# Optimization experiments

Measured on AMD Instinct MI355X. Metric: run time of the kernel, lower is better.

## Reference

```python
import jax, jax.numpy as jnp
import numpy as np

B, S, D = 2, 1024, 512
G, H, QKD, VD = 8, 8, 64, 64
FFOUT = D

def setup_inputs() -> dict:
    key = jax.random.key(0)
    ks = jax.random.split(key, 7)
    def lin(kw, fan_in, fan_out):
        lim = 1.0 / np.sqrt(fan_in)
        kw1, kw2 = jax.random.split(kw)
        w = jax.random.uniform(kw1, (fan_in, fan_out), jnp.float32, -lim, lim)
        b = jax.random.uniform(kw2, (fan_out,), jnp.float32, -lim, lim)
        return w, b
    x = jax.random.normal(ks[0], (B, S, D), jnp.float32)
    Wq_w, Wq_b = lin(ks[1], D, H * G * QKD)
    Wkv_w, Wkv_b = lin(ks[2], D, G * (QKD + VD))
    Wz_w, Wz_b = lin(ks[3], VD * H * G, FFOUT)
    return {"x": x, "Wq_w": Wq_w, "Wq_b": Wq_b, "Wkv_w": Wkv_w,
            "Wkv_b": Wkv_b, "Wz_w": Wz_w, "Wz_b": Wz_b}

def reference(x, Wq_w, Wq_b, Wkv_w, Wkv_b, Wz_w, Wz_b):
    # m defaults to x (cross-attention path of GQA with m=None)
    m = x
    scale = 1.0 / np.sqrt(QKD)
    q = (x @ Wq_w + Wq_b).reshape(B, S, G, H, QKD)          # [b,s,g,h,d]
    kv = m @ Wkv_w + Wkv_b                                   # [b,S,g*(qk+v)]
    k = kv[..., : G * QKD].reshape(B, S, G, QKD)             # [b,S,g,d]
    v = kv[..., G * QKD :].reshape(B, S, G, VD)              # [b,S,g,d]
    qk = jnp.einsum('bsghd,bSgd->bghsS', q, k)               # [b,g,h,s,S]
    # attdropout=0 -> Identity; softmax applied to scaled scores
    weight = jax.nn.softmax(qk * scale, axis=-1)
    z = jnp.einsum('bghsS,bSgd->bsghd', weight, v)           # [b,s,g,h,d]
    z = z.reshape(B, S, G * H * VD)
    out = jax.nn.leaky_relu(z @ Wz_w + Wz_b, negative_slope=0.01)
    return out
```

## Files before the change

kernel.cpp:

```cpp
#include <hip/hip_runtime.h>
#include <stdint.h>

#define B_   2
#define S_   1024
#define D_   512
#define G_   8
#define H_   8
#define QKD_ 64
#define VD_  64
#define T_   (B_ * S_)
#define QC_  (G_ * H_ * QKD_)
#define KVC_ (G_ * (QKD_ + VD_))
#define SPLITK_ 4

typedef __attribute__((ext_vector_type(8))) short short8;
typedef __attribute__((ext_vector_type(4))) float f32x4;

#if __has_builtin(__builtin_amdgcn_exp2f)
#define EXP2(x) __builtin_amdgcn_exp2f(x)
#else
#define EXP2(x) exp2f(x)
#endif

__device__ __forceinline__ unsigned short f2bf(float f) {
    unsigned u = __builtin_bit_cast(unsigned, f);
    u += 0x7FFF + ((u >> 16) & 1);
    return (unsigned short)(u >> 16);
}

__device__ __forceinline__ unsigned pk2(float lo, float hi) {
    return (unsigned)f2bf(lo) | ((unsigned)f2bf(hi) << 16);
}

__global__ __launch_bounds__(256) void f32_to_bf16_vec(
    const float* __restrict__ in, unsigned short* __restrict__ out, int n4)
{
    int i = blockIdx.x * 256 + threadIdx.x;
    if (i >= n4) return;
    float4 v = ((const float4*)in)[i];
    ushort4 o;
    o.x = f2bf(v.x); o.y = f2bf(v.y); o.z = f2bf(v.z); o.w = f2bf(v.w);
    ((ushort4*)out)[i] = o;
}

__global__ __launch_bounds__(256) void transpose_f32_bf16(
    const float* __restrict__ in, unsigned short* __restrict__ out, int K, int N)
{
    __shared__ float tile[32][33];
    int n0 = blockIdx.x * 32, k0 = blockIdx.y * 32;
    int tx = threadIdx.x & 31, ty = threadIdx.x >> 5;
    #pragma unroll
    for (int i = 0; i < 4; i++)
        tile[ty + i * 8][tx] = in[(size_t)(k0 + ty + i * 8) * N + n0 + tx];
    __syncthreads();
    #pragma unroll
    for (int i = 0; i < 4; i++)
        out[(size_t)(n0 + ty + i * 8) * K + k0 + tx] = f2bf(tile[tx][ty + i * 8]);
}

__global__ __launch_bounds__(256) void scatter_kv(
    const unsigned short* __restrict__ KVb,
    unsigned short* __restrict__ Kb, unsigned short* __restrict__ Vtb)
{
    int idx = blockIdx.x * 256 + threadIdx.x;
    if (idx >= T_ * KVC_) return;
    int t = idx >> 10, c = idx & 1023;
    int b = t >> 10, s = t & 1023;
    unsigned short v = KVb[idx];
    if (c < G_ * QKD_) {
        int g = c >> 6, d = c & 63;
        Kb[((size_t)(b * G_ + g) * S_ + s) * 64 + d] = v;
    } else {
        int c2 = c - G_ * QKD_;
        int g = c2 >> 6, d = c2 & 63;
        Vtb[((size_t)(b * G_ + g) * 64 + d) * S_ + s] = v;
    }
}

template <int OUT_MODE>
__global__ __launch_bounds__(256) void gemm_bt(
    const unsigned short* __restrict__ A,
    const unsigned short* __restrict__ Bt,
    const float* __restrict__ bias,
    void* __restrict__ Cout,
    int M, int N, int Kst, int Klen)
{
    constexpr int BM = 128, BN = 128, BK = 32, LDT = 40;
    __shared__ __attribute__((aligned(16))) unsigned short As[BM * LDT];
    __shared__ __attribute__((aligned(16))) unsigned short Bs[BN * LDT];
    const int tid = threadIdx.x;
    const int m0 = blockIdx.y * BM, n0 = blockIdx.x * BN;
    const int kz = blockIdx.z;
    const int koff = kz * Klen;
    const int lane = tid & 63, w = tid >> 6;
    const int wm = w >> 1, wn = w & 1;
    const int cl = lane & 15, gr = lane >> 4;

    f32x4 acc[4][4];
    #pragma unroll
    for (int i = 0; i < 4; i++)
        #pragma unroll
        for (int j = 0; j < 4; j++) acc[i][j] = {0.f, 0.f, 0.f, 0.f};

    const int o0 = tid * 16;
    const int row0 = o0 >> 6, ce0 = (o0 & 63) >> 1;
    const int o1 = o0 + 4096;
    const int row1 = o1 >> 6, ce1 = (o1 & 63) >> 1;

    const int nkt = Klen / BK;
    for (int kt = 0; kt < nkt; kt++) {
        const int k0 = koff + kt * BK;
        int4 a0 = *(const int4*)(A + (size_t)(m0 + row0) * Kst + k0 + ce0);
        int4 a1 = *(const int4*)(A + (size_t)(m0 + row1) * Kst + k0 + ce1);
        int4 b0 = *(const int4*)(Bt + (size_t)(n0 + row0) * Kst + k0 + ce0);
        int4 b1 = *(const int4*)(Bt + (size_t)(n0 + row1) * Kst + k0 + ce1);
        __syncthreads();
        *(int4*)&As[row0 * LDT + ce0] = a0;
        *(int4*)&As[row1 * LDT + ce1] = a1;
        *(int4*)&Bs[row0 * LDT + ce0] = b0;
        *(int4*)&Bs[row1 * LDT + ce1] = b1;
        __syncthreads();
        short8 af[4], bfr[4];
        #pragma unroll
        for (int mr = 0; mr < 4; mr++)
            af[mr] = *(const short8*)&As[(wm * 64 + mr * 16 + cl) * LDT + gr * 8];
        #pragma unroll
        for (int nr = 0; nr < 4; nr++)
            bfr[nr] = *(const short8*)&Bs[(wn * 64 + nr * 16 + cl) * LDT + gr * 8];
        #pragma unroll
        for (int mr = 0; mr < 4; mr++)
            #pragma unroll
            for (int nr = 0; nr < 4; nr++)
                acc[mr][nr] = __builtin_amdgcn_mfma_f32_16x16x32_bf16(
                    af[mr], bfr[nr], acc[mr][nr], 0, 0, 0);
    }

    #pragma unroll
    for (int mr = 0; mr < 4; mr++) {
        #pragma unroll
        for (int nr = 0; nr < 4; nr++) {
            const int col = n0 + wn * 64 + nr * 16 + cl;
            const float bv = (OUT_MODE == 2) ? 0.f : bias[col];
            #pragma unroll
            for (int j = 0; j < 4; j++) {
                const int row = m0 + wm * 64 + mr * 16 + gr * 4 + j;
                float v = acc[mr][nr][j] + bv;
                if (OUT_MODE == 0) {
                    ((unsigned short*)Cout)[(size_t)row * N + col] = f2bf(v);
                } else if (OUT_MODE == 1) {
                    v = v > 0.f ? v : 0.01f * v;
                    ((float*)Cout)[(size_t)row * N + col] = v;
                } else {
                    ((float*)Cout)[(size_t)kz * M * N + (size_t)row * N + col] = v;
                }
            }
        }
    }
}

__global__ __launch_bounds__(256) void reduce_splitk(
    const float* __restrict__ part, const float* __restrict__ bias,
    float* __restrict__ out, int n4)
{
    int i = blockIdx.x * 256 + threadIdx.x;
    if (i >= n4) return;
    const float4* p = (const float4*)part;
    float4 s = p[i];
    #pragma unroll
    for (int k = 1; k < SPLITK_; k++) {
        float4 t = p[(size_t)k * n4 + i];
        s.x += t.x; s.y += t.y; s.z += t.z; s.w += t.w;
    }
    float4 bv = ((const float4*)bias)[i & (D_ / 4 - 1)];
    s.x += bv.x; s.y += bv.y; s.z += bv.z; s.w += bv.w;
    s.x = s.x > 0.f ? s.x : 0.01f * s.x;
    s.y = s.y > 0.f ? s.y : 0.01f * s.y;
    s.z = s.z > 0.f ? s.z : 0.01f * s.z;
    s.w = s.w > 0.f ? s.w : 0.01f * s.w;
    ((float4*)out)[i] = s;
}

__global__ __launch_bounds__(256) void attn_kernel(
    const unsigned short* __restrict__ Qb,
    const unsigned short* __restrict__ Kb,
    const unsigned short* __restrict__ Vtb,
    unsigned short* __restrict__ Zb)
{
    __shared__ __attribute__((aligned(16))) unsigned short KT[2][64 * 64];
    __shared__ __attribute__((aligned(16))) unsigned short VT[2][64 * 64];

    const int tid = threadIdx.x;
    const int w = tid >> 6, lane = tid & 63;
    const int cl = lane & 15, gr = (lane >> 4) & 3;
    const int bid = blockIdx.x;
    const int qt = bid & 15, head = bid >> 4;
    const int b = head >> 6, gh = head & 63;
    const int g = gh >> 3;
    const int qrow0 = qt * 64 + w * 16;

    const unsigned short* Qp =
        Qb + (size_t)(b * S_ + qrow0 + cl) * QC_ + gh * 64 + gr * 8;
    const short8 q0 = *(const short8*)(Qp);
    const short8 q1 = *(const short8*)(Qp + 32);

    const unsigned short* Khead = Kb + (size_t)(b * G_ + g) * (S_ * 64);
    const unsigned short* Vhead = Vtb + (size_t)(b * G_ + g) * (64 * S_);

    const int ko = tid * 16;
    const int kr0 = ko >> 7, kc = ko & 127;
    const int kr1 = kr0 + 32;
    const int kw0 = kr0 * 128 + (kc ^ ((kr0 & 7) << 4));
    const int kw1 = kr1 * 128 + (kc ^ ((kr1 & 7) << 4));
    const int vd = tid >> 2, vg = tid & 3;
    const int vw_a = vd * 128 + ((vg * 16) ^ ((vd & 7) << 4));
    const int vw_b = vd * 128 + (((vg + 4) * 16) ^ ((vd & 7) << 4));

    char* const kt0 = (char*)&KT[0][0];
    char* const kt1 = (char*)&KT[1][0];
    char* const vt0 = (char*)&VT[0][0];
    char* const vt1 = (char*)&VT[1][0];

    const int sw = (cl & 7) << 4;
    const int cA = (gr * 16) ^ sw;
    const int cB = (64 + gr * 16) ^ sw;

    const float C = 0.18033688011112042f;
    float m = -1e30f, l = 0.f;
    f32x4 acc[4];
    #pragma unroll
    for (int d = 0; d < 4; d++) acc[d] = {0.f, 0.f, 0.f, 0.f};

    int4 skA, skB;
    uint2 sv0, sv1, sv2, sv3;

#define LOADS(key0_)                                                          \
    {                                                                         \
        const int _k0 = (key0_);                                              \
        skA = *(const int4*)(Khead + (size_t)(_k0 + kr0) * 64 + (kc >> 1));   \
        skB = *(const int4*)(Khead + (size_t)(_k0 + kr1) * 64 + (kc >> 1));   \
        const unsigned short* _vr = Vhead + (size_t)vd * S_ + _k0;            \
        sv0 = *(const uint2*)(_vr + vg * 4);                                  \
        sv1 = *(const uint2*)(_vr + 16 + vg * 4);                             \
        sv2 = *(const uint2*)(_vr + 32 + vg * 4);                             \
        sv3 = *(const uint2*)(_vr + 48 + vg * 4);                             \
    }
#define WRITES(kt_, vt_)                                                      \
    {                                                                         \
        *(int4*)((kt_) + kw0) = skA;                                          \
        *(int4*)((kt_) + kw1) = skB;                                          \
        *(int4*)((vt_) + vw_a) =                                              \
            make_int4((int)sv0.x, (int)sv0.y, (int)sv1.x, (int)sv1.y);        \
        *(int4*)((vt_) + vw_b) =                                              \
            make_int4((int)sv2.x, (int)sv2.y, (int)sv3.x, (int)sv3.y);        \
    }

    LOADS(0);
    WRITES(kt0, vt0);

    for (int kt = 0; kt < S_ / 64; kt++) {
        const int sel = kt & 1;
        __syncthreads();
        if (kt + 1 < S_ / 64) LOADS((kt + 1) * 64);

        const char* kbuf = sel ? kt1 : kt0;
        const char* vbuf = sel ? vt1 : vt0;

        f32x4 s[4];
        #pragma unroll
        for (int bb = 0; bb < 4; bb++) {
            const char* kr = kbuf + (bb * 16 + cl) * 128;
            short8 kf0 = *(const short8*)(kr + cA);
            short8 kf1 = *(const short8*)(kr + cB);
            f32x4 z = {0.f, 0.f, 0.f, 0.f};
            z = __builtin_amdgcn_mfma_f32_16x16x32_bf16(kf0, q0, z, 0, 0, 0);
            z = __builtin_amdgcn_mfma_f32_16x16x32_bf16(kf1, q1, z, 0, 0, 0);
            s[bb] = z;
        }

        float t0 = fmaxf(fmaxf(s[0][0], s[0][1]), fmaxf(s[0][2], s[0][3]));
        float t1 = fmaxf(fmaxf(s[1][0], s[1][1]), fmaxf(s[1][2], s[1][3]));
        float t2 = fmaxf(fmaxf(s[2][0], s[2][1]), fmaxf(s[2][2], s[2][3]));
        float t3 = fmaxf(fmaxf(s[3][0], s[3][1]), fmaxf(s[3][2], s[3][3]));
        float mx = fmaxf(fmaxf(t0, t1), fmaxf(t2, t3));
        mx = fmaxf(mx, __shfl_xor(mx, 16));
        mx = fmaxf(mx, __shfl_xor(mx, 32));

        if (!__all(mx - m <= 44.3614f)) {
            const float mn = fmaxf(m, mx);
            const float corr = EXP2((m - mn) * C);
            m = mn;
            l *= corr;
            #pragma unroll
            for (int d = 0; d < 4; d++) acc[d] *= corr;
        }
        const float mC = m * C;

        float p[4][4];
        #pragma unroll
        for (int bb = 0; bb < 4; bb++)
            #pragma unroll
            for (int j = 0; j < 4; j++)
                p[bb][j] = EXP2(fmaf(s[bb][j], C, -mC));

        float a0 = (p[0][0] + p[0][1]) + (p[0][2] + p[0][3]);
        float a1 = (p[1][0] + p[1][1]) + (p[1][2] + p[1][3]);
        float a2 = (p[2][0] + p[2][1]) + (p[2][2] + p[2][3]);
        float a3 = (p[3][0] + p[3][1]) + (p[3][2] + p[3][3]);
        l += (a0 + a1) + (a2 + a3);

        union { unsigned u[4]; short8 v; } pb0, pb1;
        asm("v_cvt_pk_bf16_f32 %0, %1, %2" : "=v"(pb0.u[0]) : "v"(p[0][0]), "v"(p[0][1]));
        asm("v_cvt_pk_bf16_f32 %0, %1, %2" : "=v"(pb0.u[1]) : "v"(p[0][2]), "v"(p[0][3]));
        asm("v_cvt_pk_bf16_f32 %0, %1, %2" : "=v"(pb0.u[2]) : "v"(p[1][0]), "v"(p[1][1]));
        asm("v_cvt_pk_bf16_f32 %0, %1, %2" : "=v"(pb0.u[3]) : "v"(p[1][2]), "v"(p[1][3]));
        asm("v_cvt_pk_bf16_f32 %0, %1, %2" : "=v"(pb1.u[0]) : "v"(p[2][0]), "v"(p[2][1]));
        asm("v_cvt_pk_bf16_f32 %0, %1, %2" : "=v"(pb1.u[1]) : "v"(p[2][2]), "v"(p[2][3]));
        asm("v_cvt_pk_bf16_f32 %0, %1, %2" : "=v"(pb1.u[2]) : "v"(p[3][0]), "v"(p[3][1]));
        asm("v_cvt_pk_bf16_f32 %0, %1, %2" : "=v"(pb1.u[3]) : "v"(p[3][2]), "v"(p[3][3]));

        #pragma unroll
        for (int db = 0; db < 4; db++) {
            const char* vr = vbuf + (db * 16 + cl) * 128;
            short8 vf0 = *(const short8*)(vr + cA);
            short8 vf1 = *(const short8*)(vr + cB);
            acc[db] = __builtin_amdgcn_mfma_f32_16x16x32_bf16(vf0, pb0.v, acc[db], 0, 0, 0);
            acc[db] = __builtin_amdgcn_mfma_f32_16x16x32_bf16(vf1, pb1.v, acc[db], 0, 0, 0);
        }

        if (kt + 1 < S_ / 64) {
            if (sel) { WRITES(kt0, vt0); } else { WRITES(kt1, vt1); }
        }
    }
#undef LOADS
#undef WRITES

    l += __shfl_xor(l, 16);
    l += __shfl_xor(l, 32);
    const float rl = 1.0f / l;
    unsigned short* zrow = Zb + (size_t)(b * S_ + qrow0 + cl) * QC_ + gh * 64;
    #pragma unroll
    for (int db = 0; db < 4; db++) {
        uint2 o;
        o.x = pk2(acc[db][0] * rl, acc[db][1] * rl);
        o.y = pk2(acc[db][2] * rl, acc[db][3] * rl);
        *(uint2*)(zrow + db * 16 + gr * 4) = o;
    }
}

extern "C" void kernel_launch(void* const* d_in, const int* in_sizes, int n_in,
                              void* d_out, int out_size, void* d_ws, size_t ws_size,
                              hipStream_t stream)
{
    const float* x     = (const float*)d_in[0];
    const float* Wq_w  = (const float*)d_in[1];
    const float* Wq_b  = (const float*)d_in[2];
    const float* Wkv_w = (const float*)d_in[3];
    const float* Wkv_b = (const float*)d_in[4];
    const float* Wz_w  = (const float*)d_in[5];
    const float* Wz_b  = (const float*)d_in[6];
    float* out = (float*)d_out;

    unsigned short* ws   = (unsigned short*)d_ws;
    unsigned short* xb   = ws;
    unsigned short* WqT  = xb   + (size_t)T_ * D_;
    unsigned short* WkvT = WqT  + (size_t)QC_ * D_;
    unsigned short* WzT  = WkvT + (size_t)KVC_ * D_;
    unsigned short* Qb   = WzT  + (size_t)D_ * QC_;
    unsigned short* KVb  = Qb   + (size_t)T_ * QC_;
    unsigned short* Kb   = KVb  + (size_t)T_ * KVC_;
    unsigned short* Vtb  = Kb   + (size_t)B_ * G_ * S_ * 64;
    unsigned short* Zb   = Vtb  + (size_t)B_ * G_ * 64 * S_;
    float* Pp = (float*)Qb;

    f32_to_bf16_vec<<<(T_ * D_ / 4 + 255) / 256, 256, 0, stream>>>(x, xb, T_ * D_ / 4);
    transpose_f32_bf16<<<dim3(QC_ / 32, D_ / 32), 256, 0, stream>>>(Wq_w, WqT, D_, QC_);
    transpose_f32_bf16<<<dim3(KVC_ / 32, D_ / 32), 256, 0, stream>>>(Wkv_w, WkvT, D_, KVC_);
    transpose_f32_bf16<<<dim3(D_ / 32, QC_ / 32), 256, 0, stream>>>(Wz_w, WzT, QC_, D_);

    gemm_bt<0><<<dim3(QC_ / 128, T_ / 128), 256, 0, stream>>>(
        xb, WqT, Wq_b, Qb, T_, QC_, D_, D_);
    gemm_bt<0><<<dim3(KVC_ / 128, T_ / 128), 256, 0, stream>>>(
        xb, WkvT, Wkv_b, KVb, T_, KVC_, D_, D_);
    scatter_kv<<<(T_ * KVC_ + 255) / 256, 256, 0, stream>>>(KVb, Kb, Vtb);
    attn_kernel<<<B_ * G_ * H_ * (S_ / 64), 256, 0, stream>>>(Qb, Kb, Vtb, Zb);

    gemm_bt<2><<<dim3(D_ / 128, T_ / 128, SPLITK_), 256, 0, stream>>>(
        Zb, WzT, nullptr, Pp, T_, D_, QC_, QC_ / SPLITK_);
    reduce_splitk<<<(T_ * D_ / 4 + 255) / 256, 256, 0, stream>>>(
        Pp, Wz_b, out, T_ * D_ / 4);
}
```

Before: 220.9 us.

## Fuse Q and KV projections with scatter epilogue; widen attention blocks to 128 queries

Merges the Q and KV projection GEMMs into one launch over concatenated weights. The epilogue writes K and transposed V straight into their attention layouts, which removes the intermediate KV buffer and the separate scatter kernel. The attention kernel now uses 512-thread blocks covering 128 query rows, so each K/V tile staged in shared memory serves twice as many queries and each thread does half the staging loads. The scattered bf16 stores in the GEMM epilogue are uncoalesced, especially for V-transpose, and the larger blocks reduce the number of blocks per CU.

```diff
diff --git a/kernel.cpp b/kernel.cpp
--- a/kernel.cpp
+++ b/kernel.cpp
@@ -58,31 +58,15 @@
         out[(size_t)(n0 + ty + i * 8) * K + k0 + tx] = f2bf(tile[tx][ty + i * 8]);
 }
 
-__global__ __launch_bounds__(256) void scatter_kv(
-    const unsigned short* __restrict__ KVb,
-    unsigned short* __restrict__ Kb, unsigned short* __restrict__ Vtb)
-{
-    int idx = blockIdx.x * 256 + threadIdx.x;
-    if (idx >= T_ * KVC_) return;
-    int t = idx >> 10, c = idx & 1023;
-    int b = t >> 10, s = t & 1023;
-    unsigned short v = KVb[idx];
-    if (c < G_ * QKD_) {
-        int g = c >> 6, d = c & 63;
-        Kb[((size_t)(b * G_ + g) * S_ + s) * 64 + d] = v;
-    } else {
-        int c2 = c - G_ * QKD_;
-        int g = c2 >> 6, d = c2 & 63;
-        Vtb[((size_t)(b * G_ + g) * 64 + d) * S_ + s] = v;
-    }
-}
-
 template <int OUT_MODE>
 __global__ __launch_bounds__(256) void gemm_bt(
     const unsigned short* __restrict__ A,
     const unsigned short* __restrict__ Bt,
     const float* __restrict__ bias,
+    const float* __restrict__ bias2,
     void* __restrict__ Cout,
+    unsigned short* __restrict__ Kbo,
+    unsigned short* __restrict__ Vto,
     int M, int N, int Kst, int Klen)
 {
     constexpr int BM = 128, BN = 128, BK = 32, LDT = 40;
@@ -140,18 +124,31 @@
         #pragma unroll
         for (int nr = 0; nr < 4; nr++) {
             const int col = n0 + wn * 64 + nr * 16 + cl;
-            const float bv = (OUT_MODE == 2) ? 0.f : bias[col];
+            float bv = 0.f;
+            if (OUT_MODE == 3)
+                bv = (col < QC_) ? bias[col] : bias2[col - QC_];
             #pragma unroll
             for (int j = 0; j < 4; j++) {
                 const int row = m0 + wm * 64 + mr * 16 + gr * 4 + j;
                 float v = acc[mr][nr][j] + bv;
-                if (OUT_MODE == 0) {
-                    ((unsigned short*)Cout)[(size_t)row * N + col] = f2bf(v);
-                } else if (OUT_MODE == 1) {
-                    v = v > 0.f ? v : 0.01f * v;
-                    ((float*)Cout)[(size_t)row * N + col] = v;
+                if (OUT_MODE == 2) {
+                    ((float*)Cout)[(size_t)kz * M * N + (size_t)row * N + col] = v;
                 } else {
-                    ((float*)Cout)[(size_t)kz * M * N + (size_t)row * N + col] = v;
+                    const unsigned short h = f2bf(v);
+                    if (col < QC_) {
+                        ((unsigned short*)Cout)[(size_t)row * QC_ + col] = h;
+                    } else {
+                        const int c2 = col - QC_;
+                        const int bb = row >> 10, s = row & 1023;
+                        if (c2 < G_ * QKD_) {
+                            const int g = c2 >> 6, d = c2 & 63;
+                            Kbo[((size_t)((bb << 3) + g) * 1024 + s) * 64 + d] = h;
+                        } else {
+                            const int c3 = c2 - G_ * QKD_;
+                            const int g = c3 >> 6, d = c3 & 63;
+                            Vto[((size_t)((bb << 3) + g) * 64 + d) * 1024 + s] = h;
+                        }
+                    }
                 }
             }
         }
@@ -180,7 +177,7 @@
     ((float4*)out)[i] = s;
 }
 
-__global__ __launch_bounds__(256) void attn_kernel(
+__global__ __launch_bounds__(512) void attn_kernel(
     const unsigned short* __restrict__ Qb,
     const unsigned short* __restrict__ Kb,
     const unsigned short* __restrict__ Vtb,
@@ -193,10 +190,10 @@
     const int w = tid >> 6, lane = tid & 63;
     const int cl = lane & 15, gr = (lane >> 4) & 3;
     const int bid = blockIdx.x;
-    const int qt = bid & 15, head = bid >> 4;
+    const int qt = bid & 7, head = bid >> 3;
     const int b = head >> 6, gh = head & 63;
     const int g = gh >> 3;
-    const int qrow0 = qt * 64 + w * 16;
+    const int qrow0 = qt * 128 + w * 16;
 
     const unsigned short* Qp =
         Qb + (size_t)(b * S_ + qrow0 + cl) * QC_ + gh * 64 + gr * 8;
@@ -206,14 +203,11 @@
     const unsigned short* Khead = Kb + (size_t)(b * G_ + g) * (S_ * 64);
     const unsigned short* Vhead = Vtb + (size_t)(b * G_ + g) * (64 * S_);
 
-    const int ko = tid * 16;
-    const int kr0 = ko >> 7, kc = ko & 127;
-    const int kr1 = kr0 + 32;
-    const int kw0 = kr0 * 128 + (kc ^ ((kr0 & 7) << 4));
-    const int kw1 = kr1 * 128 + (kc ^ ((kr1 & 7) << 4));
-    const int vd = tid >> 2, vg = tid & 3;
-    const int vw_a = vd * 128 + ((vg * 16) ^ ((vd & 7) << 4));
-    const int vw_b = vd * 128 + (((vg + 4) * 16) ^ ((vd & 7) << 4));
+    const int kr = tid >> 3, kc = (tid & 7) * 16;
+    const int kw = kr * 128 + (kc ^ ((kr & 7) << 4));
+    const int vd = tid >> 3, vg = tid & 7;
+    const int vbase = (vg & 3) * 4 + (vg >> 2) * 32;
+    const int vw = vd * 128 + ((vg * 16) ^ ((vd & 7) << 4));
 
     char* const kt0 = (char*)&KT[0][0];
     char* const kt1 = (char*)&KT[1][0];
@@ -230,28 +224,22 @@
     #pragma unroll
     for (int d = 0; d < 4; d++) acc[d] = {0.f, 0.f, 0.f, 0.f};
 
-    int4 skA, skB;
-    uint2 sv0, sv1, sv2, sv3;
+    int4 skA;
+    uint2 sv0, sv1;
 
 #define LOADS(key0_)                                                          \
     {                                                                         \
         const int _k0 = (key0_);                                              \
-        skA = *(const int4*)(Khead + (size_t)(_k0 + kr0) * 64 + (kc >> 1));   \
-        skB = *(const int4*)(Khead + (size_t)(_k0 + kr1) * 64 + (kc >> 1));   \
-        const unsigned short* _vr = Vhead + (size_t)vd * S_ + _k0;            \
-        sv0 = *(const uint2*)(_vr + vg * 4);                                  \
-        sv1 = *(const uint2*)(_vr + 16 + vg * 4);                             \
-        sv2 = *(const uint2*)(_vr + 32 + vg * 4);                             \
-        sv3 = *(const uint2*)(_vr + 48 + vg * 4);                             \
+        skA = *(const int4*)(Khead + (size_t)(_k0 + kr) * 64 + (kc >> 1));    \
+        const unsigned short* _vr = Vhead + (size_t)vd * S_ + _k0 + vbase;    \
+        sv0 = *(const uint2*)(_vr);                                           \
+        sv1 = *(const uint2*)(_vr + 16);                                      \
     }
 #define WRITES(kt_, vt_)                                                      \
     {                                                                         \
-        *(int4*)((kt_) + kw0) = skA;                                          \
-        *(int4*)((kt_) + kw1) = skB;                                          \
-        *(int4*)((vt_) + vw_a) =                                              \
+        *(int4*)((kt_) + kw) = skA;                                           \
+        *(int4*)((vt_) + vw) =                                                \
             make_int4((int)sv0.x, (int)sv0.y, (int)sv1.x, (int)sv1.y);        \
-        *(int4*)((vt_) + vw_b) =                                              \
-            make_int4((int)sv2.x, (int)sv2.y, (int)sv3.x, (int)sv3.y);        \
     }
 
     LOADS(0);
@@ -268,9 +256,9 @@
         f32x4 s[4];
         #pragma unroll
         for (int bb = 0; bb < 4; bb++) {
-            const char* kr = kbuf + (bb * 16 + cl) * 128;
-            short8 kf0 = *(const short8*)(kr + cA);
-            short8 kf1 = *(const short8*)(kr + cB);
+            const char* kr_ = kbuf + (bb * 16 + cl) * 128;
+            short8 kf0 = *(const short8*)(kr_ + cA);
+            short8 kf1 = *(const short8*)(kr_ + cB);
             f32x4 z = {0.f, 0.f, 0.f, 0.f};
             z = __builtin_amdgcn_mfma_f32_16x16x32_bf16(kf0, q0, z, 0, 0, 0);
             z = __builtin_amdgcn_mfma_f32_16x16x32_bf16(kf1, q1, z, 0, 0, 0);
@@ -366,8 +354,7 @@
     unsigned short* WkvT = WqT  + (size_t)QC_ * D_;
     unsigned short* WzT  = WkvT + (size_t)KVC_ * D_;
     unsigned short* Qb   = WzT  + (size_t)D_ * QC_;
-    unsigned short* KVb  = Qb   + (size_t)T_ * QC_;
-    unsigned short* Kb   = KVb  + (size_t)T_ * KVC_;
+    unsigned short* Kb   = Qb   + (size_t)T_ * QC_;
     unsigned short* Vtb  = Kb   + (size_t)B_ * G_ * S_ * 64;
     unsigned short* Zb   = Vtb  + (size_t)B_ * G_ * 64 * S_;
     float* Pp = (float*)Qb;
@@ -377,15 +364,13 @@
     transpose_f32_bf16<<<dim3(KVC_ / 32, D_ / 32), 256, 0, stream>>>(Wkv_w, WkvT, D_, KVC_);
     transpose_f32_bf16<<<dim3(D_ / 32, QC_ / 32), 256, 0, stream>>>(Wz_w, WzT, QC_, D_);
 
-    gemm_bt<0><<<dim3(QC_ / 128, T_ / 128), 256, 0, stream>>>(
-        xb, WqT, Wq_b, Qb, T_, QC_, D_, D_);
-    gemm_bt<0><<<dim3(KVC_ / 128, T_ / 128), 256, 0, stream>>>(
-        xb, WkvT, Wkv_b, KVb, T_, KVC_, D_, D_);
-    scatter_kv<<<(T_ * KVC_ + 255) / 256, 256, 0, stream>>>(KVb, Kb, Vtb);
-    attn_kernel<<<B_ * G_ * H_ * (S_ / 64), 256, 0, stream>>>(Qb, Kb, Vtb, Zb);
+    gemm_bt<3><<<dim3((QC_ + KVC_) / 128, T_ / 128), 256, 0, stream>>>(
+        xb, WqT, Wq_b, Wkv_b, Qb, Kb, Vtb, T_, QC_ + KVC_, D_, D_);
+
+    attn_kernel<<<B_ * G_ * H_ * (S_ / 128), 512, 0, stream>>>(Qb, Kb, Vtb, Zb);
 
     gemm_bt<2><<<dim3(D_ / 128, T_ / 128, SPLITK_), 256, 0, stream>>>(
-        Zb, WzT, nullptr, Pp, T_, D_, QC_, QC_ / SPLITK_);
+        Zb, WzT, nullptr, nullptr, Pp, nullptr, nullptr, T_, D_, QC_, QC_ / SPLITK_);
     reduce_splitk<<<(T_ * D_ / 4 + 255) / 256, 256, 0, stream>>>(
         Pp, Wz_b, out, T_ * D_ / 4);
 }
```

Result: faster. 192.7 us (-12.7%).
